# Kernel tuning notes

Hardware: AMD Instinct MI355X
Metric: run time of the kernel (lower is better)

The kernel has to match this reference:

```python
import jax, jax.numpy as jnp
import numpy as np

T, D, R, C, L = 4096, 512, 32, 32, 2  # time, input, trace, context, num_blocks
NEG_SLOPE = 0.01
EPS = 1e-5  # eqx LayerNorm default


def _layernorm(x, g, b):
    m = jnp.mean(x, -1, keepdims=True)
    v = jnp.var(x, -1, keepdims=True)
    return g * (x - m) * jax.lax.rsqrt(v + EPS) + b


def _ffa_scan(a, b, pre, s0, start):
    # a:[R], b:[C], pre:[T,R,C] real>=0, s0:[1,R,C] complex64, start:[T] bool
    ab = jax.lax.complex(jnp.broadcast_to(-jnp.abs(a)[:, None], (R, C)),
                         jnp.broadcast_to(b[None, :], (R, C)))  # log decay+rotation
    ts = jnp.concatenate([jnp.zeros((1,), jnp.float32), jnp.ones((T,), jnp.float32)])
    vals = jnp.concatenate([s0, pre.astype(jnp.complex64)], axis=0)  # [T+1,R,C]
    rst = jnp.concatenate([jnp.zeros((1,), bool), start])

    def op(l, r):
        tl, sl, dl = l
        tr, sr, dr = r
        decay = jnp.exp(ab[None, :, :] * tr[:, None, None])  # gamma^{t_r}
        s = jnp.where(dr[:, None, None], sr, sr + sl * decay)
        t = jnp.where(dr, tr, tl + tr)
        return (t, s, dl | dr)

    _, states, _ = jax.lax.associative_scan(op, (ts, vals, rst))
    return states[1:]  # [T,R,C]


def _forward(x, start_b, state_real, state_imag, Wt, Wc, a, b,
             W0, b0, g0, beta0, W1, b1, g1, beta1):
    h = x
    z = x
    for i in range(L):
        tr = h @ Wt[i].T  # [T,R]
        ct = h @ Wc[i].T  # [T,R] (source maps context proj to trace_size too; R==C)
        pre = jnp.abs(tr[:, :, None] * ct[:, None, :])  # [T,R,C] outer product
        pre = pre / (1e-8 + jnp.sum(pre, axis=(-2, -1), keepdims=True))
        s0 = jax.lax.complex(state_real[i], state_imag[i])  # [1,R,C]
        states = _ffa_scan(a[i], b[i], pre, s0, start_b)
        s = states.reshape(T, R * C)
        mag = jnp.log1p(jnp.abs(s))
        ang = jnp.angle(s)
        scaled = jnp.concatenate([mag * jnp.sin(ang), mag * jnp.cos(ang)], axis=-1)  # [T,2RC]
        z = jax.nn.leaky_relu(_layernorm(scaled @ W0[i].T + b0[i], g0[i], beta0[i]), NEG_SLOPE)
        z = jax.nn.leaky_relu(_layernorm(z @ W1[i].T + b1[i], g1[i], beta1[i]), NEG_SLOPE)
        h = h + z  # residual feeds next block; NSFFM returns last block's z
    return z


def setup_inputs() -> dict:
    key = jax.random.key(0)
    ks = jax.random.split(key, 8)
    x = jax.random.normal(ks[0], (T, D), jnp.float32)
    start = jax.random.randint(ks[1], (T,), 0, 2).astype(jnp.int32)
    next_done = jax.random.randint(ks[2], (T,), 0, 2).astype(jnp.int32)
    Wt = jax.random.normal(ks[3], (L, R, D), jnp.float32) / np.sqrt(D)
    Wc = jax.random.normal(ks[4], (L, R, D), jnp.float32) / np.sqrt(D)
    # ffa.init: a = linspace decays, b = log-spaced angular frequencies
    a = jnp.broadcast_to(jnp.linspace(1e-6, 0.5, R, dtype=jnp.float32)[None], (L, R)).copy()
    b = jnp.broadcast_to((2 * jnp.pi / jnp.exp(jnp.linspace(np.log(1.0), np.log(1024.0), C))).astype(jnp.float32)[None], (L, C)).copy()
    W0 = jax.random.normal(ks[5], (L, D, 2 * R * C), jnp.float32) * 0.01  # default_init scale=0.01
    W1 = jax.random.normal(ks[6], (L, D, D), jnp.float32) / np.sqrt(D)
    return {
        'x': x, 'start': start, 'next_done': next_done,
        'state_real': jnp.zeros((L, 1, R, C), jnp.float32),
        'state_imag': jnp.zeros((L, 1, R, C), jnp.float32),
        'Wt': Wt, 'Wc': Wc, 'a': a, 'b': b,
        'W0': W0, 'b0': jnp.zeros((L, D), jnp.float32),
        'g0': jnp.ones((L, D), jnp.float32), 'beta0': jnp.zeros((L, D), jnp.float32),
        'W1': W1, 'b1': jnp.zeros((L, D), jnp.float32),
        'g1': jnp.ones((L, D), jnp.float32), 'beta1': jnp.zeros((L, D), jnp.float32),
    }


def reference(x, start, next_done, state_real, state_imag, Wt, Wc, a, b,
              W0, b0, g0, beta0, W1, b1, g1, beta1):
    del next_done  # not used in the scan math (kept for interface parity)
    start_b = start.astype(bool)
    return _forward(x, start_b, state_real, state_imag, Wt, Wc, a, b,
                    W0, b0, g0, beta0, W1, b1, g1, beta1)
```

## Files before the change

### kernel.cpp

```cpp
#include <hip/hip_runtime.h>
#include <math.h>

#define TT 4096
#define DD 512
#define RR 32
#define CC 32
#define RC 1024
#define LL 2
#define CHUNK 32
#define NCHUNK 128
#define NEG_SLOPE 0.01f
#define LN_EPS 1e-5f

typedef __attribute__((ext_vector_type(8))) __bf16 bf16x8;
typedef __attribute__((ext_vector_type(4))) float f32x4;

__device__ __forceinline__ unsigned short f2bf(float f) {
    unsigned int u = __builtin_bit_cast(unsigned int, f);
    u += 0x7fffu + ((u >> 16) & 1u);
    return (unsigned short)(u >> 16);
}

#define NX4  524288
#define NW04 524288
#define NW14 131072
#define NCV  (NX4 + NW04 + NW14)
#define NPK  16384
__global__ __launch_bounds__(256) void setup_kernel(const float4* __restrict__ x,
                                                    const float4* __restrict__ W0,
                                                    const float4* __restrict__ W1,
                                                    const float* __restrict__ Wt,
                                                    const float* __restrict__ Wc,
                                                    ushort4* __restrict__ xb,
                                                    ushort4* __restrict__ W0b,
                                                    ushort4* __restrict__ W1b,
                                                    ushort4* __restrict__ Wtc) {
    int i = blockIdx.x * 256 + threadIdx.x;
    float4 v;
    ushort4* dst;
    int j;
    if (i < NCV) {
        const float4* src;
        if (i < NX4) { src = x; dst = xb; j = i; }
        else if (i < NX4 + NW04) { src = W0; dst = W0b; j = i - NX4; }
        else { src = W1; dst = W1b; j = i - NX4 - NW04; }
        v = src[j];
    } else {
        int ii = i - NCV;
        if (ii >= NPK) return;
        int e = ii * 4;
        int l = e >> 15;
        int r = (e >> 9) & 63;
        int k = e & 511;
        v = (r < 32) ? *(const float4*)&Wt[((size_t)l * 32 + r) * 512 + k]
                     : *(const float4*)&Wc[((size_t)l * 32 + (r - 32)) * 512 + k];
        dst = Wtc; j = ii;
    }
    ushort4 o;
    o.x = f2bf(v.x); o.y = f2bf(v.y); o.z = f2bf(v.z); o.w = f2bf(v.w);
    dst[j] = o;
}

__global__ __launch_bounds__(256) void proj_denom_kernel(const unsigned short* __restrict__ A,
                                                         const unsigned short* __restrict__ B,
                                                         float* __restrict__ tcabs) {
    __shared__ __align__(16) unsigned short As[64 * 32];
    __shared__ __align__(16) unsigned short Bs[64 * 32];
    const int tid = threadIdx.x;
    const int w = tid >> 6, lane = tid & 63;
    const int bm = blockIdx.x * 64;
    const int K = 512;
    const int srow = tid >> 2;
    const int sl = tid & 3;
    const int sswz = (sl ^ ((srow >> 1) & 3)) * 8;
    const unsigned short* gA = A + (size_t)(bm + srow) * K + sl * 8;
    const unsigned short* gB = B + (size_t)srow * K + sl * 8;
    const int wA = srow * 32 + sswz;
    const int wB = srow * 32 + sswz;
    const int fr = lane & 15, hi = lane >> 4;
    const int kslot = hi ^ ((fr >> 1) & 3);
    f32x4 acc0 = {}, acc1 = {}, acc2 = {}, acc3 = {};

    uint4 va = *(const uint4*)gA;
    uint4 vb = *(const uint4*)gB;
    for (int k0 = 0; k0 < K; k0 += 32) {
        __syncthreads();
        *(uint4*)&As[wA] = va;
        *(uint4*)&Bs[wB] = vb;
        __syncthreads();
        if (k0 + 32 < K) {
            va = *(const uint4*)(gA + k0 + 32);
            vb = *(const uint4*)(gB + k0 + 32);
        }
        const int arow = w * 16 + fr;
        bf16x8 af = *(const bf16x8*)&As[arow * 32 + kslot * 8];
        bf16x8 b0 = *(const bf16x8*)&Bs[(0 * 16 + fr) * 32 + kslot * 8];
        bf16x8 b1 = *(const bf16x8*)&Bs[(1 * 16 + fr) * 32 + kslot * 8];
        bf16x8 b2 = *(const bf16x8*)&Bs[(2 * 16 + fr) * 32 + kslot * 8];
        bf16x8 b3 = *(const bf16x8*)&Bs[(3 * 16 + fr) * 32 + kslot * 8];
        acc0 = __builtin_amdgcn_mfma_f32_16x16x32_bf16(af, b0, acc0, 0, 0, 0);
        acc1 = __builtin_amdgcn_mfma_f32_16x16x32_bf16(af, b1, acc1, 0, 0, 0);
        acc2 = __builtin_amdgcn_mfma_f32_16x16x32_bf16(af, b2, acc2, 0, 0, 0);
        acc3 = __builtin_amdgcn_mfma_f32_16x16x32_bf16(af, b3, acc3, 0, 0, 0);
    }
#pragma unroll
    for (int q = 0; q < 4; ++q) {
        float a0 = fabsf(acc0[q]), a1 = fabsf(acc1[q]);
        float a2 = fabsf(acc2[q]), a3 = fabsf(acc3[q]);
        float st = a0 + a1, sc = a2 + a3;
        st += __shfl_xor(st, 1); sc += __shfl_xor(sc, 1);
        st += __shfl_xor(st, 2); sc += __shfl_xor(sc, 2);
        st += __shfl_xor(st, 4); sc += __shfl_xor(sc, 4);
        st += __shfl_xor(st, 8); sc += __shfl_xor(sc, 8);
        float inv = 1.f / (1e-8f + st * sc);
        size_t rb = (size_t)(bm + w * 16 + hi * 4 + q) * 64;
        tcabs[rb + fr]      = a0 * inv;
        tcabs[rb + fr + 16] = a1 * inv;
        tcabs[rb + fr + 32] = a2;
        tcabs[rb + fr + 48] = a3;
    }
}

__global__ __launch_bounds__(256) void scan_pass1(const float* __restrict__ tcabs,
                                                  const int* __restrict__ start,
                                                  const float* __restrict__ a,
                                                  const float* __restrict__ b,
                                                  float4* __restrict__ ab4) {
    int tid = blockIdx.x * 256 + threadIdx.x;
    int rc = tid & (RC - 1);
    int chunk = tid >> 10;
    int r = rc >> 5, c = rc & 31;
    float e = expf(-fabsf(a[r]));
    float gr = e * cosf(b[c]);
    float gi = e * sinf(b[c]);
    float alr = 1.f, ali = 0.f, ber = 0.f, bei = 0.f;
    int t0 = chunk * CHUNK;
    for (int j = 0; j < CHUNK; ++j) {
        int t = t0 + j;
        float pre = tcabs[t * 64 + r] * tcabs[t * 64 + 32 + c];
        if (start[t]) {
            alr = 0.f; ali = 0.f; ber = pre; bei = 0.f;
        } else {
            float nbr = pre + gr * ber - gi * bei;
            float nbi =       gr * bei + gi * ber;
            float nar = gr * alr - gi * ali;
            float nai = gr * ali + gi * alr;
            ber = nbr; bei = nbi; alr = nar; ali = nai;
        }
    }
    ab4[chunk * RC + rc] = make_float4(alr, ali, ber, bei);
}

__global__ __launch_bounds__(256) void scan_pass2f(const float* __restrict__ tcabs,
                                                   const float4* __restrict__ ab4,
                                                   const int* __restrict__ start,
                                                   const float* __restrict__ a,
                                                   const float* __restrict__ b,
                                                   const float* __restrict__ s0r,
                                                   const float* __restrict__ s0i,
                                                   unsigned short* __restrict__ scaled) {
    int bx = blockIdx.x;
    int chunk = bx >> 2;
    int rc = (bx & 3) * 256 + threadIdx.x;
    int r = rc >> 5, c = rc & 31;
    float e = expf(-fabsf(a[r]));
    float gr = e * cosf(b[c]);
    float gi = e * sinf(b[c]);
    float sr = s0r[rc], si = s0i[rc];
    int j = 0;
    for (; j + 8 <= chunk; j += 8) {
        float4 buf[8];
#pragma unroll
        for (int u = 0; u < 8; ++u) buf[u] = ab4[(j + u) * RC + rc];
#pragma unroll
        for (int u = 0; u < 8; ++u) {
            float nsr = buf[u].z + buf[u].x * sr - buf[u].y * si;
            float nsi = buf[u].w + buf[u].x * si + buf[u].y * sr;
            sr = nsr; si = nsi;
        }
    }
    for (; j < chunk; ++j) {
        float4 ab = ab4[j * RC + rc];
        float nsr = ab.z + ab.x * sr - ab.y * si;
        float nsi = ab.w + ab.x * si + ab.y * sr;
        sr = nsr; si = nsi;
    }
    int t0 = chunk * CHUNK;
    for (int jj = 0; jj < CHUNK; ++jj) {
        int t = t0 + jj;
        float pre = tcabs[t * 64 + r] * tcabs[t * 64 + 32 + c];
        if (start[t]) {
            sr = pre; si = 0.f;
        } else {
            float nsr = pre + gr * sr - gi * si;
            float nsi =       gr * si + gi * sr;
            sr = nsr; si = nsi;
        }
        float m = sqrtf(sr * sr + si * si);
        float mag = log1pf(m);
        float f = (m > 0.f) ? (mag / m) : 0.f;
        scaled[(size_t)t * 2048 + rc]        = f2bf(si * f);
        scaled[(size_t)t * 2048 + 1024 + rc] = f2bf(sr * f);
    }
}

template <int K, int N, int SPLITK>
__global__ __launch_bounds__(256) void gemm_bt_mfma(const unsigned short* __restrict__ A,
                                                    const unsigned short* __restrict__ B,
                                                    float* __restrict__ Cm) {
    __shared__ __align__(16) unsigned short As[128 * 32];
    __shared__ __align__(16) unsigned short Bs[64 * 32];
    const int tid = threadIdx.x;
    const int w = tid >> 6, lane = tid & 63;
    const int nwg = gridDim.x * gridDim.y * gridDim.z;
    const int id = blockIdx.x + gridDim.x * (blockIdx.y + gridDim.y * blockIdx.z);
    const int lid = (id & 7) * (nwg >> 3) + (id >> 3);
    const int bxs = lid % gridDim.x;
    const int t2 = lid / gridDim.x;
    const int bys = t2 % gridDim.y;
    const int bzs = t2 / gridDim.y;
    const int bm = bys * 128, bn = bxs * 64;
    const int kbeg = bzs * (K / SPLITK);
    const int kend = kbeg + (K / SPLITK);
    const int wr = w >> 1, wc = w & 1;
    const int lr = lane >> 2;
    const int sl = lane & 3;
    const int swz_st = sl ^ ((lr >> 1) & 3);
    const size_t a_row0 = (size_t)(bm + w * 16 + lr);
    const size_t a_row1 = (size_t)(bm + 64 + w * 16 + lr);
    const size_t b_row  = (size_t)(bn + w * 16 + lr);
    const unsigned short* gA0 = A + a_row0 * K + sl * 8;
    const unsigned short* gA1 = A + a_row1 * K + sl * 8;
    const unsigned short* gB  = B + b_row  * K + sl * 8;
    const int wA0 = (w * 16 + lr) * 32 + swz_st * 8;
    const int wA1 = (64 + w * 16 + lr) * 32 + swz_st * 8;
    const int wB  = (w * 16 + lr) * 32 + swz_st * 8;
    const int fr = lane & 15, hi = lane >> 4;
    const int kslot = hi ^ ((fr >> 1) & 3);
    f32x4 acc[4][2] = {};

    uint4 va0 = *(const uint4*)(gA0 + kbeg);
    uint4 va1 = *(const uint4*)(gA1 + kbeg);
    uint4 vb  = *(const uint4*)(gB  + kbeg);
    for (int k0 = kbeg; k0 < kend; k0 += 32) {
        __syncthreads();
        *(uint4*)&As[wA0] = va0;
        *(uint4*)&As[wA1] = va1;
        *(uint4*)&Bs[wB]  = vb;
        __syncthreads();
        if (k0 + 32 < kend) {
            va0 = *(const uint4*)(gA0 + k0 + 32);
            va1 = *(const uint4*)(gA1 + k0 + 32);
            vb  = *(const uint4*)(gB  + k0 + 32);
        }
        bf16x8 af[4], bfv[2];
#pragma unroll
        for (int mi = 0; mi < 4; ++mi) {
            int row = wr * 64 + mi * 16 + fr;
            af[mi] = *(const bf16x8*)&As[row * 32 + kslot * 8];
        }
#pragma unroll
        for (int ni = 0; ni < 2; ++ni) {
            int row = wc * 32 + ni * 16 + fr;
            bfv[ni] = *(const bf16x8*)&Bs[row * 32 + kslot * 8];
        }
#pragma unroll
        for (int mi = 0; mi < 4; ++mi)
#pragma unroll
            for (int ni = 0; ni < 2; ++ni)
                acc[mi][ni] = __builtin_amdgcn_mfma_f32_16x16x32_bf16(
                    af[mi], bfv[ni], acc[mi][ni], 0, 0, 0);
    }
    float* Cz = Cm + (size_t)bzs * TT * N;
    const int ccol0 = bn + wc * 32 + fr;
    const int crow0 = bm + wr * 64 + hi * 4;
#pragma unroll
    for (int ni = 0; ni < 2; ++ni) {
        int col = ccol0 + ni * 16;
#pragma unroll
        for (int mi = 0; mi < 4; ++mi)
#pragma unroll
            for (int q = 0; q < 4; ++q)
                Cz[(size_t)(crow0 + mi * 16 + q) * N + col] = acc[mi][ni][q];
    }
}

__global__ __launch_bounds__(256) void ln_lrelu_kernel(const float* __restrict__ y0,
                                                       const float* __restrict__ y1,
                                                       const float* __restrict__ badd,
                                                       const float* __restrict__ g,
                                                       const float* __restrict__ be,
                                                       unsigned short* __restrict__ zb,
                                                       const float* __restrict__ res,
                                                       unsigned short* __restrict__ hbf,
                                                       float* __restrict__ fout) {
    int t = blockIdx.x;
    int tid = threadIdx.x;
    size_t base = (size_t)t * 512;
    float v0 = y0[base + tid] + y1[base + tid] + badd[tid];
    float v1 = y0[base + 256 + tid] + y1[base + 256 + tid] + badd[256 + tid];
    float s = v0 + v1, ss = v0 * v0 + v1 * v1;
#pragma unroll
    for (int o = 32; o > 0; o >>= 1) {
        s  += __shfl_down(s, o);
        ss += __shfl_down(ss, o);
    }
    __shared__ float sh[8];
    __shared__ float mrs[2];
    int wid = tid >> 6, lane = tid & 63;
    if (lane == 0) { sh[wid] = s; sh[4 + wid] = ss; }
    __syncthreads();
    if (tid == 0) {
        float S = sh[0] + sh[1] + sh[2] + sh[3];
        float SS = sh[4] + sh[5] + sh[6] + sh[7];
        float m = S * (1.f / 512.f);
        float var = SS * (1.f / 512.f) - m * m;
        mrs[0] = m;
        mrs[1] = rsqrtf(var + LN_EPS);
    }
    __syncthreads();
    float m = mrs[0], rs = mrs[1];
    float z0 = g[tid] * (v0 - m) * rs + be[tid];
    float z1 = g[256 + tid] * (v1 - m) * rs + be[256 + tid];
    z0 = (z0 > 0.f) ? z0 : NEG_SLOPE * z0;
    z1 = (z1 > 0.f) ? z1 : NEG_SLOPE * z1;
    if (zb)   { zb[base + tid] = f2bf(z0); zb[base + 256 + tid] = f2bf(z1); }
    if (hbf) {
        float h0 = (res ? res[base + tid] : 0.f) + z0;
        float h1 = (res ? res[base + 256 + tid] : 0.f) + z1;
        hbf[base + tid] = f2bf(h0);
        hbf[base + 256 + tid] = f2bf(h1);
    }
    if (fout) { fout[base + tid] = z0; fout[base + 256 + tid] = z1; }
}

extern "C" void kernel_launch(void* const* d_in, const int* in_sizes, int n_in,
                              void* d_out, int out_size, void* d_ws, size_t ws_size,
                              hipStream_t stream) {
    const float* x     = (const float*)d_in[0];
    const int*   start = (const int*)d_in[1];
    const float* s0r = (const float*)d_in[3];
    const float* s0i = (const float*)d_in[4];
    const float* Wt  = (const float*)d_in[5];
    const float* Wc  = (const float*)d_in[6];
    const float* a   = (const float*)d_in[7];
    const float* b   = (const float*)d_in[8];
    const float* W0  = (const float*)d_in[9];
    const float* b0  = (const float*)d_in[10];
    const float* g0  = (const float*)d_in[11];
    const float* be0 = (const float*)d_in[12];
    const float* W1  = (const float*)d_in[13];
    const float* b1  = (const float*)d_in[14];
    const float* g1  = (const float*)d_in[15];
    const float* be1 = (const float*)d_in[16];
    float* out = (float*)d_out;
    float* ws  = (float*)d_ws;

    float* p = ws;
    float* tcabs  = p; p += 262144;
    float4* ab4   = (float4*)p; p += 524288;
    unsigned short* scaled = (unsigned short*)p; p += 4194304;
    float* ybufp  = p; p += 4194304;
    unsigned short* zbuf_bf = (unsigned short*)p; p += 1048576;
    unsigned short* x_bf    = (unsigned short*)p; p += 1048576;
    unsigned short* h_bf    = (unsigned short*)p; p += 1048576;
    unsigned short* Wtcbf   = (unsigned short*)p; p += 32768;
    unsigned short* W0bf    = (unsigned short*)p; p += 1048576;
    unsigned short* W1bf    = (unsigned short*)p; p += 262144;

    setup_kernel<<<(NCV + NPK + 255) / 256, 256, 0, stream>>>(
        (const float4*)x, (const float4*)W0, (const float4*)W1, Wt, Wc,
        (ushort4*)x_bf, (ushort4*)W0bf, (ushort4*)W1bf, (ushort4*)Wtcbf);

    for (int i = 0; i < LL; ++i) {
        const unsigned short* hb = (i == 0) ? x_bf : h_bf;
        proj_denom_kernel<<<64, 256, 0, stream>>>(
            hb, Wtcbf + (size_t)i * 64 * 512, tcabs);
        scan_pass1<<<NCHUNK * RC / 256, 256, 0, stream>>>(
            tcabs, start, a + i * RR, b + i * CC, ab4);
        scan_pass2f<<<NCHUNK * 4, 256, 0, stream>>>(
            tcabs, ab4, start, a + i * RR, b + i * CC,
            s0r + i * RC, s0i + i * RC, scaled);
        gemm_bt_mfma<2048, 512, 2><<<dim3(8, 32, 2), 256, 0, stream>>>(
            scaled, W0bf + (size_t)i * 512 * 2048, ybufp);
        ln_lrelu_kernel<<<TT, 256, 0, stream>>>(
            ybufp, ybufp + (size_t)TT * 512, b0 + i * DD, g0 + i * DD, be0 + i * DD,
            zbuf_bf, nullptr, nullptr, nullptr);
        gemm_bt_mfma<512, 512, 2><<<dim3(8, 32, 2), 256, 0, stream>>>(
            zbuf_bf, W1bf + (size_t)i * 512 * 512, ybufp);
        ln_lrelu_kernel<<<TT, 256, 0, stream>>>(
            ybufp, ybufp + (size_t)TT * 512, b1 + i * DD, g1 + i * DD, be1 + i * DD,
            nullptr,
            (i < LL - 1) ? x : nullptr,
            (i < LL - 1) ? h_bf : nullptr,
            (i == LL - 1) ? out : nullptr);
    }
}
```

Measured before the change: 202.4 us.

## Widen GEMM tiles to 128x128 and raise split-K to four partials

The bf16 MFMA GEMM tile grows from 128x64 to 128x128, so each wave computes a 64x64 sub-tile with a 4x4 accumulator array. This reuses each A fragment across more MFMAs. To keep the grid size at 512 workgroups, split-K goes from 2 to 4, and the LayerNorm kernel now sums four fp32 partial buffers. The cost is double the partial-output traffic and workspace, plus more registers per thread, which may lower occupancy.

Result: slower. 214.6 us (+6.0%).

```diff
diff --git a/kernel.cpp b/kernel.cpp
--- a/kernel.cpp
+++ b/kernel.cpp
@@ -209,7 +209,7 @@
                                                     const unsigned short* __restrict__ B,
                                                     float* __restrict__ Cm) {
     __shared__ __align__(16) unsigned short As[128 * 32];
-    __shared__ __align__(16) unsigned short Bs[64 * 32];
+    __shared__ __align__(16) unsigned short Bs[128 * 32];
     const int tid = threadIdx.x;
     const int w = tid >> 6, lane = tid & 63;
     const int nwg = gridDim.x * gridDim.y * gridDim.z;
@@ -219,63 +219,67 @@
     const int t2 = lid / gridDim.x;
     const int bys = t2 % gridDim.y;
     const int bzs = t2 / gridDim.y;
-    const int bm = bys * 128, bn = bxs * 64;
+    const int bm = bys * 128, bn = bxs * 128;
     const int kbeg = bzs * (K / SPLITK);
     const int kend = kbeg + (K / SPLITK);
     const int wr = w >> 1, wc = w & 1;
-    const int lr = lane >> 2;
-    const int sl = lane & 3;
-    const int swz_st = sl ^ ((lr >> 1) & 3);
-    const size_t a_row0 = (size_t)(bm + w * 16 + lr);
-    const size_t a_row1 = (size_t)(bm + 64 + w * 16 + lr);
-    const size_t b_row  = (size_t)(bn + w * 16 + lr);
-    const unsigned short* gA0 = A + a_row0 * K + sl * 8;
-    const unsigned short* gA1 = A + a_row1 * K + sl * 8;
-    const unsigned short* gB  = B + b_row  * K + sl * 8;
-    const int wA0 = (w * 16 + lr) * 32 + swz_st * 8;
-    const int wA1 = (64 + w * 16 + lr) * 32 + swz_st * 8;
-    const int wB  = (w * 16 + lr) * 32 + swz_st * 8;
+    const int r0 = tid >> 2;
+    const int r1 = 64 + (tid >> 2);
+    const int sl = tid & 3;
+    const int swz0 = (sl ^ ((r0 >> 1) & 3)) * 8;
+    const int swz1 = (sl ^ ((r1 >> 1) & 3)) * 8;
+    const unsigned short* gA0 = A + (size_t)(bm + r0) * K + sl * 8;
+    const unsigned short* gA1 = A + (size_t)(bm + r1) * K + sl * 8;
+    const unsigned short* gB0 = B + (size_t)(bn + r0) * K + sl * 8;
+    const unsigned short* gB1 = B + (size_t)(bn + r1) * K + sl * 8;
+    const int wA0 = r0 * 32 + swz0;
+    const int wA1 = r1 * 32 + swz1;
+    const int wB0 = r0 * 32 + swz0;
+    const int wB1 = r1 * 32 + swz1;
     const int fr = lane & 15, hi = lane >> 4;
     const int kslot = hi ^ ((fr >> 1) & 3);
-    f32x4 acc[4][2] = {};
+    f32x4 acc[4][4] = {};
 
     uint4 va0 = *(const uint4*)(gA0 + kbeg);
     uint4 va1 = *(const uint4*)(gA1 + kbeg);
-    uint4 vb  = *(const uint4*)(gB  + kbeg);
+    uint4 vb0 = *(const uint4*)(gB0 + kbeg);
+    uint4 vb1 = *(const uint4*)(gB1 + kbeg);
     for (int k0 = kbeg; k0 < kend; k0 += 32) {
         __syncthreads();
         *(uint4*)&As[wA0] = va0;
         *(uint4*)&As[wA1] = va1;
-        *(uint4*)&Bs[wB]  = vb;
+        *(uint4*)&Bs[wB0] = vb0;
+        *(uint4*)&Bs[wB1] = vb1;
         __syncthreads();
         if (k0 + 32 < kend) {
             va0 = *(const uint4*)(gA0 + k0 + 32);
             va1 = *(const uint4*)(gA1 + k0 + 32);
-            vb  = *(const uint4*)(gB  + k0 + 32);
-        }
-        bf16x8 af[4], bfv[2];
+            vb0 = *(const uint4*)(gB0 + k0 + 32);
+            vb1 = *(const uint4*)(gB1 + k0 + 32);
+        }
+        bf16x8 af[4], bfv[4];
 #pragma unroll
         for (int mi = 0; mi < 4; ++mi) {
             int row = wr * 64 + mi * 16 + fr;
             af[mi] = *(const bf16x8*)&As[row * 32 + kslot * 8];
         }
 #pragma unroll
-        for (int ni = 0; ni < 2; ++ni) {
-            int row = wc * 32 + ni * 16 + fr;
+        for (int ni = 0; ni < 4; ++ni) {
+            int row = wc * 64 + ni * 16 + fr;
             bfv[ni] = *(const bf16x8*)&Bs[row * 32 + kslot * 8];
         }
 #pragma unroll
         for (int mi = 0; mi < 4; ++mi)
 #pragma unroll
-            for (int ni = 0; ni < 2; ++ni)
+            for (int ni = 0; ni < 4; ++ni)
                 acc[mi][ni] = __builtin_amdgcn_mfma_f32_16x16x32_bf16(
                     af[mi], bfv[ni], acc[mi][ni], 0, 0, 0);
     }
     float* Cz = Cm + (size_t)bzs * TT * N;
-    const int ccol0 = bn + wc * 32 + fr;
+    const int ccol0 = bn + wc * 64 + fr;
     const int crow0 = bm + wr * 64 + hi * 4;
 #pragma unroll
-    for (int ni = 0; ni < 2; ++ni) {
+    for (int ni = 0; ni < 4; ++ni) {
         int col = ccol0 + ni * 16;
 #pragma unroll
         for (int mi = 0; mi < 4; ++mi)
@@ -285,8 +289,7 @@
     }
 }
 
-__global__ __launch_bounds__(256) void ln_lrelu_kernel(const float* __restrict__ y0,
-                                                       const float* __restrict__ y1,
+__global__ __launch_bounds__(256) void ln_lrelu_kernel(const float* __restrict__ yb,
                                                        const float* __restrict__ badd,
                                                        const float* __restrict__ g,
                                                        const float* __restrict__ be,
@@ -297,8 +300,12 @@
     int t = blockIdx.x;
     int tid = threadIdx.x;
     size_t base = (size_t)t * 512;
-    float v0 = y0[base + tid] + y1[base + tid] + badd[tid];
-    float v1 = y0[base + 256 + tid] + y1[base + 256 + tid] + badd[256 + tid];
+    const size_t PS = (size_t)TT * 512;
+    float v0 = yb[base + tid] + yb[PS + base + tid]
+             + yb[2 * PS + base + tid] + yb[3 * PS + base + tid] + badd[tid];
+    float v1 = yb[base + 256 + tid] + yb[PS + base + 256 + tid]
+             + yb[2 * PS + base + 256 + tid] + yb[3 * PS + base + 256 + tid]
+             + badd[256 + tid];
     float s = v0 + v1, ss = v0 * v0 + v1 * v1;
 #pragma unroll
     for (int o = 32; o > 0; o >>= 1) {
@@ -360,7 +367,7 @@
     float* tcabs  = p; p += 262144;
     float4* ab4   = (float4*)p; p += 524288;
     unsigned short* scaled = (unsigned short*)p; p += 4194304;
-    float* ybufp  = p; p += 4194304;
+    float* ybufp  = p; p += 8388608;
     unsigned short* zbuf_bf = (unsigned short*)p; p += 1048576;
     unsigned short* x_bf    = (unsigned short*)p; p += 1048576;
     unsigned short* h_bf    = (unsigned short*)p; p += 1048576;
@@ -381,15 +388,15 @@
         scan_pass2f<<<NCHUNK * 4, 256, 0, stream>>>(
             tcabs, ab4, start, a + i * RR, b + i * CC,
             s0r + i * RC, s0i + i * RC, scaled);
-        gemm_bt_mfma<2048, 512, 2><<<dim3(8, 32, 2), 256, 0, stream>>>(
+        gemm_bt_mfma<2048, 512, 4><<<dim3(4, 32, 4), 256, 0, stream>>>(
             scaled, W0bf + (size_t)i * 512 * 2048, ybufp);
         ln_lrelu_kernel<<<TT, 256, 0, stream>>>(
-            ybufp, ybufp + (size_t)TT * 512, b0 + i * DD, g0 + i * DD, be0 + i * DD,
+            ybufp, b0 + i * DD, g0 + i * DD, be0 + i * DD,
             zbuf_bf, nullptr, nullptr, nullptr);
-        gemm_bt_mfma<512, 512, 2><<<dim3(8, 32, 2), 256, 0, stream>>>(
+        gemm_bt_mfma<512, 512, 4><<<dim3(4, 32, 4), 256, 0, stream>>>(
             zbuf_bf, W1bf + (size_t)i * 512 * 512, ybufp);
         ln_lrelu_kernel<<<TT, 256, 0, stream>>>(
-            ybufp, ybufp + (size_t)TT * 512, b1 + i * DD, g1 + i * DD, be1 + i * DD,
+            ybufp, b1 + i * DD, g1 + i * DD, be1 + i * DD,
             nullptr,
             (i < LL - 1) ? x : nullptr,
             (i < LL - 1) ? h_bf : nullptr,
```
